# Optimization experiments

Hardware: AMD Instinct MI355X
Metric: run time of the kernel (lower is better)

Reference implementation:

```python
import jax, jax.numpy as jnp
import numpy as np

D_QK = 32  # out_channels // 8


def conv1x1(x, w, b):
    # x: [B,C,H,W], w: [O,C], b: [O] -> [B,O,H,W]
    return jnp.einsum('bchw,oc->bohw', x, w) + b[None, :, None, None]


def setup_inputs() -> dict:
    key = jax.random.key(0)
    ks = jax.random.split(key, 10)
    B, C, H, W = 4, 256, 64, 64
    in_ch, out_ch, attn_ch = 512, 256, 256
    s_in = 1.0 / np.sqrt(in_ch)
    s_at = 1.0 / np.sqrt(attn_ch)
    return {
        'ef': jax.random.normal(ks[0], (B, C, H, W), jnp.float32),
        'sf': jax.random.normal(ks[1], (B, C, H, W), jnp.float32),
        'Attn': jax.random.normal(ks[2], (B, attn_ch, H, W), jnp.float32),
        'Qw': jax.random.uniform(ks[3], (D_QK, in_ch), jnp.float32, -s_in, s_in),
        'Qb': jax.random.uniform(ks[4], (D_QK,), jnp.float32, -s_in, s_in),
        'Kw': jax.random.uniform(ks[5], (D_QK, attn_ch), jnp.float32, -s_at, s_at),
        'Kb': jax.random.uniform(ks[6], (D_QK,), jnp.float32, -s_at, s_at),
        'Vw': jax.random.uniform(ks[7], (out_ch, in_ch), jnp.float32, -s_in, s_in),
        'Vb': jax.random.uniform(ks[8], (out_ch,), jnp.float32, -s_in, s_in),
        'gamma': jnp.ones((1,), jnp.float32) * 0.25,
    }


def reference(ef, sf, Attn, Qw, Qb, Kw, Kb, Vw, Vb, gamma):
    B, C, H, W = ef.shape
    N = H * W
    x = jnp.concatenate((ef, sf), axis=1)  # [B, 2C, H, W]
    q = conv1x1(x, Qw, Qb).reshape(B, D_QK, N)         # [B, d, N]
    k = conv1x1(Attn, Kw, Kb).reshape(B, D_QK, N)      # [B, d, N]
    # scores[b, m, n] = sum_d q[b, d, m] * k[b, d, n]  (no 1/sqrt(d) scale)
    scores = jnp.einsum('bdm,bdn->bmn', q, k)
    attn = jax.nn.softmax(scores, axis=-1)             # [B, N, N]
    v = conv1x1(x, Vw, Vb).reshape(B, C, N)            # [B, C, N]
    # out[b, c, m] = sum_n v[b, c, n] * attn[b, m, n]
    out = jnp.einsum('bcn,bmn->bcm', v, attn).reshape(B, C, H, W)
    return gamma[0] * out + ef
```

## Files before the change

kernel.cpp:

```cpp
#include <hip/hip_runtime.h>
#include <hip/hip_bf16.h>

typedef short bf16x8 __attribute__((ext_vector_type(8)));
typedef float f32x4 __attribute__((ext_vector_type(4)));

#define MFMA16(a, b, c) __builtin_amdgcn_mfma_f32_16x16x32_bf16(a, b, c, 0, 0, 0)

#define NB 4
#define NC 256
#define NSP 4096
#define LOG2E 1.4426950408889634f

__device__ __forceinline__ unsigned short f2bf(float f) {
    return (unsigned short)((__float_as_uint(f) + 0x8000u) >> 16);
}
__device__ __forceinline__ unsigned pk2bf(float hi, float lo) {
    return __builtin_amdgcn_perm(__float_as_uint(hi) + 0x8000u,
                                 __float_as_uint(lo) + 0x8000u, 0x07060302u);
}

__global__ __launch_bounds__(256) void prep(
    const float* __restrict__ ef, const float* __restrict__ sf,
    const float* __restrict__ attn,
    const float* __restrict__ Qw, const float* __restrict__ Kw,
    const float* __restrict__ Vw,
    unsigned short* __restrict__ xt, unsigned short* __restrict__ at,
    unsigned short* __restrict__ Qwbf, unsigned short* __restrict__ Kwbf,
    unsigned short* __restrict__ Vwbf)
{
    __shared__ float tile[64][65];
    int gid = blockIdx.x;
    int t = threadIdx.x;

    if (gid >= 3072) {
        int i = (gid - 3072) * 256 + t;
        {
            const float4* vs = (const float4*)(Vw + (size_t)i * 8);
            float4 a = vs[0], c = vs[1];
            int4 st;
            st.x = (int)pk2bf(a.y, a.x); st.y = (int)pk2bf(a.w, a.z);
            st.z = (int)pk2bf(c.y, c.x); st.w = (int)pk2bf(c.w, c.z);
            *(int4*)(Vwbf + (size_t)i * 8) = st;
        }
        if (i < 2048) {
            const float4* qs = (const float4*)(Qw + (size_t)i * 8);
            float4 a = qs[0], c = qs[1];
            int4 st;
            st.x = (int)pk2bf(a.y, a.x); st.y = (int)pk2bf(a.w, a.z);
            st.z = (int)pk2bf(c.y, c.x); st.w = (int)pk2bf(c.w, c.z);
            *(int4*)(Qwbf + (size_t)i * 8) = st;
        }
        if (i < 1024) {
            const float4* ks = (const float4*)(Kw + (size_t)i * 8);
            float4 a = ks[0], c = ks[1];
            int4 st;
            st.x = (int)pk2bf(a.y, a.x); st.y = (int)pk2bf(a.w, a.z);
            st.z = (int)pk2bf(c.y, c.x); st.w = (int)pk2bf(c.w, c.z);
            *(int4*)(Kwbf + (size_t)i * 8) = st;
        }
        return;
    }

    const float* src; unsigned short* dst;
    int mt, cdst0, CW;
    if (gid < 2048) {
        int b = gid >> 9, r = gid & 511;
        mt = r >> 3; int ct = r & 7;
        src = (ct < 4 ? ef : sf) + ((size_t)(b * NC) + (ct & 3) * 64) * NSP;
        dst = xt + (size_t)b * NSP * 512; cdst0 = ct * 64; CW = 512;
    } else {
        int g2 = gid - 2048;
        int b = g2 >> 8, r = g2 & 255;
        mt = r >> 2; int ct = r & 3;
        src = attn + ((size_t)(b * NC) + ct * 64) * NSP;
        dst = at + (size_t)b * NSP * 256; cdst0 = ct * 64; CW = 256;
    }
    int m0 = mt * 64;
    int ml = t & 63, cl = t >> 6;
#pragma unroll
    for (int r = 0; r < 16; ++r)
        tile[ml][r * 4 + cl] = src[(size_t)(r * 4 + cl) * NSP + m0 + ml];
    __syncthreads();
    int cp = t & 31, mw = t >> 5;
#pragma unroll
    for (int r = 0; r < 8; ++r) {
        int m_l = r * 8 + mw;
        float v0 = tile[m_l][2 * cp], v1 = tile[m_l][2 * cp + 1];
        *(unsigned*)(dst + (size_t)(m0 + m_l) * CW + cdst0 + 2 * cp) = pk2bf(v1, v0);
    }
}

__global__ __launch_bounds__(256, 4) void proj(
    const unsigned short* __restrict__ xt, const unsigned short* __restrict__ at,
    const unsigned short* __restrict__ Qwbf, const unsigned short* __restrict__ Kwbf,
    const unsigned short* __restrict__ Vwbf,
    const float* __restrict__ Qb, const float* __restrict__ Kb,
    const float* __restrict__ Vb,
    unsigned short* __restrict__ qws, unsigned short* __restrict__ kws,
    unsigned short* __restrict__ vws)
{
    int bi = blockIdx.x;
    int t = threadIdx.x;
    int w = t >> 6, lane = t & 63, quad = lane >> 4, l15 = lane & 15;
    f32x4 zero = {0.f, 0.f, 0.f, 0.f};

    if (bi < 256) {
        int b = bi >> 6, m = (bi & 63) * 64 + w * 16;
        f32x4 a0 = zero, a1 = zero;
        const unsigned short* xrow = xt + ((size_t)(b * NSP) + m + l15) * 512;
#pragma unroll 4
        for (int ks = 0; ks < 16; ++ks) {
            bf16x8 af = *(const bf16x8*)(xrow + ks * 32 + quad * 8);
            bf16x8 b0 = *(const bf16x8*)(Qwbf + (size_t)l15 * 512 + ks * 32 + quad * 8);
            bf16x8 b1 = *(const bf16x8*)(Qwbf + (size_t)(16 + l15) * 512 + ks * 32 + quad * 8);
            a0 = MFMA16(af, b0, a0);
            a1 = MFMA16(af, b1, a1);
        }
        float bq0 = Qb[l15], bq1 = Qb[16 + l15];
#pragma unroll
        for (int r = 0; r < 4; ++r) {
            size_t mr = (size_t)(b * NSP) + m + quad * 4 + r;
            qws[mr * 32 + l15]      = f2bf((a0[r] + bq0) * LOG2E);
            qws[mr * 32 + 16 + l15] = f2bf((a1[r] + bq1) * LOG2E);
        }
    } else if (bi < 512) {
        int r2 = bi - 256;
        int b = r2 >> 6, m = (r2 & 63) * 64 + w * 16;
        f32x4 a0 = zero, a1 = zero;
        const unsigned short* arow = at + ((size_t)(b * NSP) + m + l15) * 256;
#pragma unroll 4
        for (int ks = 0; ks < 8; ++ks) {
            bf16x8 af = *(const bf16x8*)(arow + ks * 32 + quad * 8);
            bf16x8 b0 = *(const bf16x8*)(Kwbf + (size_t)l15 * 256 + ks * 32 + quad * 8);
            bf16x8 b1 = *(const bf16x8*)(Kwbf + (size_t)(16 + l15) * 256 + ks * 32 + quad * 8);
            a0 = MFMA16(af, b0, a0);
            a1 = MFMA16(af, b1, a1);
        }
        float bk0 = Kb[l15], bk1 = Kb[16 + l15];
#pragma unroll
        for (int r = 0; r < 4; ++r) {
            size_t mr = (size_t)(b * NSP) + m + quad * 4 + r;
            kws[mr * 32 + l15]      = f2bf(a0[r] + bk0);
            kws[mr * 32 + 16 + l15] = f2bf(a1[r] + bk1);
        }
    } else {
        int r2 = bi - 512;
        int mt = r2 & 127, coh = (r2 >> 7) & 1, b = r2 >> 8;
        int m0 = mt * 32;
        int co0 = coh * 128 + w * 32;

        f32x4 acc[2][2];
        acc[0][0] = zero; acc[0][1] = zero; acc[1][0] = zero; acc[1][1] = zero;

        const unsigned short* x0 = xt + ((size_t)(b * NSP) + m0 + l15) * 512;
        const unsigned short* x1 = x0 + 16 * 512;
        const unsigned short* vw0 = Vwbf + (size_t)(co0 + l15) * 512;
        const unsigned short* vw1 = Vwbf + (size_t)(co0 + 16 + l15) * 512;
#pragma unroll 4
        for (int ks = 0; ks < 16; ++ks) {
            bf16x8 a0 = *(const bf16x8*)(x0 + ks * 32 + quad * 8);
            bf16x8 a1 = *(const bf16x8*)(x1 + ks * 32 + quad * 8);
            bf16x8 b0 = *(const bf16x8*)(vw0 + ks * 32 + quad * 8);
            bf16x8 b1 = *(const bf16x8*)(vw1 + ks * 32 + quad * 8);
            acc[0][0] = MFMA16(a0, b0, acc[0][0]);
            acc[0][1] = MFMA16(a0, b1, acc[0][1]);
            acc[1][0] = MFMA16(a1, b0, acc[1][0]);
            acc[1][1] = MFMA16(a1, b1, acc[1][1]);
        }
#pragma unroll
        for (int mi = 0; mi < 2; ++mi)
#pragma unroll
            for (int ci = 0; ci < 2; ++ci) {
                int co = co0 + ci * 16 + l15;
                float bias = Vb[co];
                unsigned short* vp = vws + ((size_t)(b * 128 + mt) * 256 + co) * 32;
#pragma unroll
                for (int r = 0; r < 4; ++r)
                    vp[2 * (quad * 4 + r) + mi] = f2bf(acc[mi][ci][r] + bias);
            }
    }
}

__global__ __launch_bounds__(512, 2) void attention(
    const unsigned short* __restrict__ qws, const unsigned short* __restrict__ kws,
    const unsigned short* __restrict__ vws, const float* __restrict__ ef,
    const float* __restrict__ gamma, float* __restrict__ out)
{
    __shared__ unsigned short Plds[2][2][64 * 72];
    __shared__ float mrg[256][68];
    __shared__ float denl[2][64];

    int t = threadIdx.x;
    int g = t >> 8, tl = t & 255;
    int w = tl >> 6, lane = tl & 63, quad = lane >> 4, l15 = lane & 15;
    int b = blockIdx.x >> 6, m0 = (blockIdx.x & 63) << 6;

    const unsigned short* kbase = kws + (size_t)(b * NSP) * 32;
    const unsigned short* vbase = vws + (size_t)(b * 128) * 8192;

    bf16x8 qf = *(const bf16x8*)(qws + ((size_t)(b * NSP) + m0 + w * 16 + l15) * 32 + quad * 8);

    f32x4 zero = {0.f, 0.f, 0.f, 0.f};
    f32x4 acc[4][4];
#pragma unroll
    for (int i = 0; i < 4; ++i)
#pragma unroll
        for (int j = 0; j < 4; ++j) acc[i][j] = zero;
    float lp0 = 0.f, lp1 = 0.f, lp2 = 0.f, lp3 = 0.f;

    int tt0 = g * 64;
    bf16x8 kf[4];
#pragma unroll
    for (int j = 0; j < 4; ++j)
        kf[j] = *(const bf16x8*)(kbase + (size_t)((tt0 + (j >> 1)) * 32 + (j & 1) * 16 + l15) * 32 + quad * 8);
    bf16x8 vf[2][4];
#pragma unroll
    for (int h = 0; h < 2; ++h)
#pragma unroll
        for (int cc = 0; cc < 4; ++cc)
            vf[h][cc] = *(const bf16x8*)(vbase + (size_t)(tt0 + h) * 8192 + (w * 64 + cc * 16 + l15) * 32 + quad * 8);

    for (int it = 0; it < 32; ++it) {
        int buf = it & 1;
        f32x4 s0 = MFMA16(qf, kf[0], zero);
        f32x4 s1 = MFMA16(qf, kf[1], zero);
        f32x4 s2 = MFMA16(qf, kf[2], zero);
        f32x4 s3 = MFMA16(qf, kf[3], zero);

        float e0[4], e1[4], e2[4], e3[4];
#pragma unroll
        for (int r = 0; r < 4; ++r) {
            e0[r] = __builtin_amdgcn_exp2f(s0[r]);
            e1[r] = __builtin_amdgcn_exp2f(s1[r]);
            e2[r] = __builtin_amdgcn_exp2f(s2[r]);
            e3[r] = __builtin_amdgcn_exp2f(s3[r]);
        }
        lp0 += (e0[0] + e1[0]) + (e2[0] + e3[0]);
        lp1 += (e0[1] + e1[1]) + (e2[1] + e3[1]);
        lp2 += (e0[2] + e1[2]) + (e2[2] + e3[2]);
        lp3 += (e0[3] + e1[3]) + (e2[3] + e3[3]);

        unsigned short* pd = &Plds[g][buf][(w * 16 + quad * 4) * 72 + 2 * l15];
#pragma unroll
        for (int r = 0; r < 4; ++r) {
            *(unsigned*)(pd + r * 72)      = pk2bf(e1[r], e0[r]);
            *(unsigned*)(pd + r * 72 + 32) = pk2bf(e3[r], e2[r]);
        }

        int itn = it + 1 < 32 ? it + 1 : 31;
        int ttn = tt0 + 2 * itn;
#pragma unroll
        for (int j = 0; j < 4; ++j)
            kf[j] = *(const bf16x8*)(kbase + (size_t)((ttn + (j >> 1)) * 32 + (j & 1) * 16 + l15) * 32 + quad * 8);
        bf16x8 vfn[2][4];
#pragma unroll
        for (int h = 0; h < 2; ++h)
#pragma unroll
            for (int cc = 0; cc < 4; ++cc)
                vfn[h][cc] = *(const bf16x8*)(vbase + (size_t)(ttn + h) * 8192 + (w * 64 + cc * 16 + l15) * 32 + quad * 8);

        __syncthreads();

#pragma unroll
        for (int h = 0; h < 2; ++h) {
            bf16x8 pa0 = *(const bf16x8*)&Plds[g][buf][(0  + l15) * 72 + h * 32 + quad * 8];
            bf16x8 pa1 = *(const bf16x8*)&Plds[g][buf][(16 + l15) * 72 + h * 32 + quad * 8];
            bf16x8 pa2 = *(const bf16x8*)&Plds[g][buf][(32 + l15) * 72 + h * 32 + quad * 8];
            bf16x8 pa3 = *(const bf16x8*)&Plds[g][buf][(48 + l15) * 72 + h * 32 + quad * 8];
#pragma unroll
            for (int cc = 0; cc < 4; ++cc) {
                acc[0][cc] = MFMA16(pa0, vf[h][cc], acc[0][cc]);
                acc[1][cc] = MFMA16(pa1, vf[h][cc], acc[1][cc]);
                acc[2][cc] = MFMA16(pa2, vf[h][cc], acc[2][cc]);
                acc[3][cc] = MFMA16(pa3, vf[h][cc], acc[3][cc]);
            }
        }
#pragma unroll
        for (int h = 0; h < 2; ++h)
#pragma unroll
            for (int cc = 0; cc < 4; ++cc) vf[h][cc] = vfn[h][cc];
    }

    lp0 += __shfl_xor(lp0, 1); lp0 += __shfl_xor(lp0, 2); lp0 += __shfl_xor(lp0, 4); lp0 += __shfl_xor(lp0, 8);
    lp1 += __shfl_xor(lp1, 1); lp1 += __shfl_xor(lp1, 2); lp1 += __shfl_xor(lp1, 4); lp1 += __shfl_xor(lp1, 8);
    lp2 += __shfl_xor(lp2, 1); lp2 += __shfl_xor(lp2, 2); lp2 += __shfl_xor(lp2, 4); lp2 += __shfl_xor(lp2, 8);
    lp3 += __shfl_xor(lp3, 1); lp3 += __shfl_xor(lp3, 2); lp3 += __shfl_xor(lp3, 4); lp3 += __shfl_xor(lp3, 8);
    if (l15 == 0) {
        int base = w * 16 + quad * 4;
        denl[g][base + 0] = lp0; denl[g][base + 1] = lp1;
        denl[g][base + 2] = lp2; denl[g][base + 3] = lp3;
    }
    if (g == 1) {
#pragma unroll
        for (int qc = 0; qc < 4; ++qc)
#pragma unroll
            for (int cc = 0; cc < 4; ++cc)
                *(f32x4*)&mrg[w * 64 + cc * 16 + l15][qc * 16 + quad * 4] = acc[qc][cc];
    }
    __syncthreads();

    if (g == 0) {
        float gam = gamma[0];
#pragma unroll
        for (int qc = 0; qc < 4; ++qc) {
            int qb = qc * 16 + quad * 4;
            float4 d0 = *(const float4*)&denl[0][qb];
            float4 d1 = *(const float4*)&denl[1][qb];
            float r0 = gam / (d0.x + d1.x), r1 = gam / (d0.y + d1.y);
            float r2 = gam / (d0.z + d1.z), r3 = gam / (d0.w + d1.w);
#pragma unroll
            for (int cc = 0; cc < 4; ++cc) {
                int ch = w * 64 + cc * 16 + l15;
                f32x4 part = *(const f32x4*)&mrg[ch][qb];
                size_t off = ((size_t)(b * NC + ch)) * NSP + m0 + qb;
                float4 e = *(const float4*)(ef + off);
                float4 o;
                o.x = (acc[qc][cc][0] + part[0]) * r0 + e.x;
                o.y = (acc[qc][cc][1] + part[1]) * r1 + e.y;
                o.z = (acc[qc][cc][2] + part[2]) * r2 + e.z;
                o.w = (acc[qc][cc][3] + part[3]) * r3 + e.w;
                *(float4*)(out + off) = o;
            }
        }
    }
}

extern "C" void kernel_launch(void* const* d_in, const int* in_sizes, int n_in,
                              void* d_out, int out_size, void* d_ws, size_t ws_size,
                              hipStream_t stream) {
    const float* ef    = (const float*)d_in[0];
    const float* sf    = (const float*)d_in[1];
    const float* attn  = (const float*)d_in[2];
    const float* Qw    = (const float*)d_in[3];
    const float* Qb    = (const float*)d_in[4];
    const float* Kw    = (const float*)d_in[5];
    const float* Kb    = (const float*)d_in[6];
    const float* Vw    = (const float*)d_in[7];
    const float* Vb    = (const float*)d_in[8];
    const float* gamma = (const float*)d_in[9];
    float* out = (float*)d_out;

    unsigned short* qws  = (unsigned short*)d_ws;
    unsigned short* kws  = qws + (size_t)4 * 4096 * 32;
    unsigned short* vws  = kws + (size_t)4 * 4096 * 32;
    unsigned short* xt   = vws + (size_t)4 * 128 * 256 * 32;
    unsigned short* at   = xt  + (size_t)4 * 4096 * 512;
    unsigned short* Qwbf = at  + (size_t)4 * 4096 * 256;
    unsigned short* Kwbf = Qwbf + 32 * 512;
    unsigned short* Vwbf = Kwbf + 32 * 256;

    hipLaunchKernelGGL(prep, dim3(3136), dim3(256), 0, stream,
                       ef, sf, attn, Qw, Kw, Vw, xt, at, Qwbf, Kwbf, Vwbf);
    hipLaunchKernelGGL(proj, dim3(1536), dim3(256), 0, stream,
                       xt, at, Qwbf, Kwbf, Vwbf, Qb, Kb, Vb, qws, kws, vws);
    hipLaunchKernelGGL(attention, dim3(256), dim3(512), 0, stream,
                       qws, kws, vws, ef, gamma, out);
}
```

Before: 198.0 us.

## Fuse input transpose and bf16 conversion into Q/K/V projection kernels

Removes the separate prep pass that transposed ef/sf/Attn into bf16 workspace buffers. The Q, K and V projection kernels now read the fp32 inputs directly, transpose and convert them through a small LDS tile, and feed MFMA. This saves a full round trip of the transposed activations through global memory. In exchange ef/sf are read twice (by proj_q and proj_v), there are more kernel launches, and the blocks are small with only 512 blocks each.

```diff
diff --git a/kernel.cpp b/kernel.cpp
--- a/kernel.cpp
+++ b/kernel.cpp
@@ -19,165 +19,181 @@
                                  __float_as_uint(lo) + 0x8000u, 0x07060302u);
 }
 
-__global__ __launch_bounds__(256) void prep(
-    const float* __restrict__ ef, const float* __restrict__ sf,
-    const float* __restrict__ attn,
+__global__ __launch_bounds__(256) void prep_w(
     const float* __restrict__ Qw, const float* __restrict__ Kw,
     const float* __restrict__ Vw,
-    unsigned short* __restrict__ xt, unsigned short* __restrict__ at,
     unsigned short* __restrict__ Qwbf, unsigned short* __restrict__ Kwbf,
     unsigned short* __restrict__ Vwbf)
 {
-    __shared__ float tile[64][65];
-    int gid = blockIdx.x;
-    int t = threadIdx.x;
-
-    if (gid >= 3072) {
-        int i = (gid - 3072) * 256 + t;
-        {
-            const float4* vs = (const float4*)(Vw + (size_t)i * 8);
-            float4 a = vs[0], c = vs[1];
-            int4 st;
-            st.x = (int)pk2bf(a.y, a.x); st.y = (int)pk2bf(a.w, a.z);
-            st.z = (int)pk2bf(c.y, c.x); st.w = (int)pk2bf(c.w, c.z);
-            *(int4*)(Vwbf + (size_t)i * 8) = st;
-        }
-        if (i < 2048) {
-            const float4* qs = (const float4*)(Qw + (size_t)i * 8);
-            float4 a = qs[0], c = qs[1];
-            int4 st;
-            st.x = (int)pk2bf(a.y, a.x); st.y = (int)pk2bf(a.w, a.z);
-            st.z = (int)pk2bf(c.y, c.x); st.w = (int)pk2bf(c.w, c.z);
-            *(int4*)(Qwbf + (size_t)i * 8) = st;
-        }
-        if (i < 1024) {
-            const float4* ks = (const float4*)(Kw + (size_t)i * 8);
-            float4 a = ks[0], c = ks[1];
-            int4 st;
-            st.x = (int)pk2bf(a.y, a.x); st.y = (int)pk2bf(a.w, a.z);
-            st.z = (int)pk2bf(c.y, c.x); st.w = (int)pk2bf(c.w, c.z);
-            *(int4*)(Kwbf + (size_t)i * 8) = st;
-        }
-        return;
-    }
-
-    const float* src; unsigned short* dst;
-    int mt, cdst0, CW;
-    if (gid < 2048) {
-        int b = gid >> 9, r = gid & 511;
-        mt = r >> 3; int ct = r & 7;
-        src = (ct < 4 ? ef : sf) + ((size_t)(b * NC) + (ct & 3) * 64) * NSP;
-        dst = xt + (size_t)b * NSP * 512; cdst0 = ct * 64; CW = 512;
-    } else {
-        int g2 = gid - 2048;
-        int b = g2 >> 8, r = g2 & 255;
-        mt = r >> 2; int ct = r & 3;
-        src = attn + ((size_t)(b * NC) + ct * 64) * NSP;
-        dst = at + (size_t)b * NSP * 256; cdst0 = ct * 64; CW = 256;
-    }
-    int m0 = mt * 64;
-    int ml = t & 63, cl = t >> 6;
-#pragma unroll
-    for (int r = 0; r < 16; ++r)
-        tile[ml][r * 4 + cl] = src[(size_t)(r * 4 + cl) * NSP + m0 + ml];
-    __syncthreads();
-    int cp = t & 31, mw = t >> 5;
-#pragma unroll
-    for (int r = 0; r < 8; ++r) {
-        int m_l = r * 8 + mw;
-        float v0 = tile[m_l][2 * cp], v1 = tile[m_l][2 * cp + 1];
-        *(unsigned*)(dst + (size_t)(m0 + m_l) * CW + cdst0 + 2 * cp) = pk2bf(v1, v0);
-    }
-}
-
-__global__ __launch_bounds__(256, 4) void proj(
-    const unsigned short* __restrict__ xt, const unsigned short* __restrict__ at,
-    const unsigned short* __restrict__ Qwbf, const unsigned short* __restrict__ Kwbf,
-    const unsigned short* __restrict__ Vwbf,
-    const float* __restrict__ Qb, const float* __restrict__ Kb,
-    const float* __restrict__ Vb,
-    unsigned short* __restrict__ qws, unsigned short* __restrict__ kws,
-    unsigned short* __restrict__ vws)
-{
-    int bi = blockIdx.x;
+    int i = blockIdx.x * 256 + threadIdx.x;
+    {
+        const float4* vs = (const float4*)(Vw + (size_t)i * 8);
+        float4 a = vs[0], c = vs[1];
+        int4 st;
+        st.x = (int)pk2bf(a.y, a.x); st.y = (int)pk2bf(a.w, a.z);
+        st.z = (int)pk2bf(c.y, c.x); st.w = (int)pk2bf(c.w, c.z);
+        *(int4*)(Vwbf + (size_t)i * 8) = st;
+    }
+    if (i < 2048) {
+        const float4* qs = (const float4*)(Qw + (size_t)i * 8);
+        float4 a = qs[0], c = qs[1];
+        int4 st;
+        st.x = (int)pk2bf(a.y, a.x); st.y = (int)pk2bf(a.w, a.z);
+        st.z = (int)pk2bf(c.y, c.x); st.w = (int)pk2bf(c.w, c.z);
+        *(int4*)(Qwbf + (size_t)i * 8) = st;
+    }
+    if (i < 1024) {
+        const float4* ks = (const float4*)(Kw + (size_t)i * 8);
+        float4 a = ks[0], c = ks[1];
+        int4 st;
+        st.x = (int)pk2bf(a.y, a.x); st.y = (int)pk2bf(a.w, a.z);
+        st.z = (int)pk2bf(c.y, c.x); st.w = (int)pk2bf(c.w, c.z);
+        *(int4*)(Kwbf + (size_t)i * 8) = st;
+    }
+}
+
+__global__ __launch_bounds__(256) void proj_q(
+    const float* __restrict__ ef, const float* __restrict__ sf,
+    const unsigned short* __restrict__ Qwbf, const float* __restrict__ Qb,
+    unsigned short* __restrict__ qws)
+{
+    __shared__ __align__(16) unsigned short xt[32][72];
+
     int t = threadIdx.x;
     int w = t >> 6, lane = t & 63, quad = lane >> 4, l15 = lane & 15;
+    int mt = blockIdx.x, b = blockIdx.y, m0 = mt * 32;
+    int ci = t & 63, sm = t >> 6;
+    int mi = w >> 1, oh = w & 1;
+
+    f32x4 acc = {0.f, 0.f, 0.f, 0.f};
+
+    for (int c = 0; c < 8; ++c) {
+        const float* src = (c < 4 ? ef : sf) +
+                           ((size_t)(b * NC) + (c & 3) * 64 + ci) * NSP + m0 + sm * 8;
+        float4 x0 = *(const float4*)src;
+        float4 x1 = *(const float4*)(src + 4);
+        __syncthreads();
+        unsigned short* xd = &xt[sm * 8][ci];
+        xd[0]   = f2bf(x0.x); xd[72]  = f2bf(x0.y);
+        xd[144] = f2bf(x0.z); xd[216] = f2bf(x0.w);
+        xd[288] = f2bf(x1.x); xd[360] = f2bf(x1.y);
+        xd[432] = f2bf(x1.z); xd[504] = f2bf(x1.w);
+        __syncthreads();
+        int ci0 = c * 64;
+#pragma unroll
+        for (int ks = 0; ks < 2; ++ks) {
+            bf16x8 a  = *(const bf16x8*)&xt[mi * 16 + l15][ks * 32 + quad * 8];
+            bf16x8 bq = *(const bf16x8*)(Qwbf + (size_t)(oh * 16 + l15) * 512 + ci0 + ks * 32 + quad * 8);
+            acc = MFMA16(a, bq, acc);
+        }
+    }
+
+    int o = oh * 16 + l15;
+    float bb = Qb[o];
+#pragma unroll
+    for (int r = 0; r < 4; ++r) {
+        int m = m0 + mi * 16 + quad * 4 + r;
+        qws[((size_t)(b * NSP) + m) * 32 + o] = f2bf((acc[r] + bb) * LOG2E);
+    }
+}
+
+__global__ __launch_bounds__(256) void proj_k(
+    const float* __restrict__ attn,
+    const unsigned short* __restrict__ Kwbf, const float* __restrict__ Kb,
+    unsigned short* __restrict__ kws)
+{
+    __shared__ __align__(16) unsigned short xt[32][72];
+
+    int t = threadIdx.x;
+    int w = t >> 6, lane = t & 63, quad = lane >> 4, l15 = lane & 15;
+    int mt = blockIdx.x, b = blockIdx.y, m0 = mt * 32;
+    int ci = t & 63, sm = t >> 6;
+    int mi = w >> 1, oh = w & 1;
+
+    f32x4 acc = {0.f, 0.f, 0.f, 0.f};
+
+    for (int c = 0; c < 4; ++c) {
+        const float* src = attn + ((size_t)(b * NC) + c * 64 + ci) * NSP + m0 + sm * 8;
+        float4 x0 = *(const float4*)src;
+        float4 x1 = *(const float4*)(src + 4);
+        __syncthreads();
+        unsigned short* xd = &xt[sm * 8][ci];
+        xd[0]   = f2bf(x0.x); xd[72]  = f2bf(x0.y);
+        xd[144] = f2bf(x0.z); xd[216] = f2bf(x0.w);
+        xd[288] = f2bf(x1.x); xd[360] = f2bf(x1.y);
+        xd[432] = f2bf(x1.z); xd[504] = f2bf(x1.w);
+        __syncthreads();
+        int ci0 = c * 64;
+#pragma unroll
+        for (int ks = 0; ks < 2; ++ks) {
+            bf16x8 a  = *(const bf16x8*)&xt[mi * 16 + l15][ks * 32 + quad * 8];
+            bf16x8 bk = *(const bf16x8*)(Kwbf + (size_t)(oh * 16 + l15) * 256 + ci0 + ks * 32 + quad * 8);
+            acc = MFMA16(a, bk, acc);
+        }
+    }
+
+    int o = oh * 16 + l15;
+    float bb = Kb[o];
+#pragma unroll
+    for (int r = 0; r < 4; ++r) {
+        int m = m0 + mi * 16 + quad * 4 + r;
+        kws[((size_t)(b * NSP) + m) * 32 + o] = f2bf(acc[r] + bb);
+    }
+}
+
+__global__ __launch_bounds__(256) void proj_v(
+    const float* __restrict__ ef, const float* __restrict__ sf,
+    const unsigned short* __restrict__ Vwbf, const float* __restrict__ Vb,
+    unsigned short* __restrict__ vws)
+{
+    __shared__ __align__(16) unsigned short xt[32][72];
+
+    int t = threadIdx.x;
+    int w = t >> 6, lane = t & 63, quad = lane >> 4, l15 = lane & 15;
+    int mt = blockIdx.x, b = blockIdx.y, m0 = mt * 32;
+    int ci = t & 63, sm = t >> 6;
+
     f32x4 zero = {0.f, 0.f, 0.f, 0.f};
-
-    if (bi < 256) {
-        int b = bi >> 6, m = (bi & 63) * 64 + w * 16;
-        f32x4 a0 = zero, a1 = zero;
-        const unsigned short* xrow = xt + ((size_t)(b * NSP) + m + l15) * 512;
-#pragma unroll 4
-        for (int ks = 0; ks < 16; ++ks) {
-            bf16x8 af = *(const bf16x8*)(xrow + ks * 32 + quad * 8);
-            bf16x8 b0 = *(const bf16x8*)(Qwbf + (size_t)l15 * 512 + ks * 32 + quad * 8);
-            bf16x8 b1 = *(const bf16x8*)(Qwbf + (size_t)(16 + l15) * 512 + ks * 32 + quad * 8);
-            a0 = MFMA16(af, b0, a0);
-            a1 = MFMA16(af, b1, a1);
-        }
-        float bq0 = Qb[l15], bq1 = Qb[16 + l15];
-#pragma unroll
-        for (int r = 0; r < 4; ++r) {
-            size_t mr = (size_t)(b * NSP) + m + quad * 4 + r;
-            qws[mr * 32 + l15]      = f2bf((a0[r] + bq0) * LOG2E);
-            qws[mr * 32 + 16 + l15] = f2bf((a1[r] + bq1) * LOG2E);
-        }
-    } else if (bi < 512) {
-        int r2 = bi - 256;
-        int b = r2 >> 6, m = (r2 & 63) * 64 + w * 16;
-        f32x4 a0 = zero, a1 = zero;
-        const unsigned short* arow = at + ((size_t)(b * NSP) + m + l15) * 256;
-#pragma unroll 4
-        for (int ks = 0; ks < 8; ++ks) {
-            bf16x8 af = *(const bf16x8*)(arow + ks * 32 + quad * 8);
-            bf16x8 b0 = *(const bf16x8*)(Kwbf + (size_t)l15 * 256 + ks * 32 + quad * 8);
-            bf16x8 b1 = *(const bf16x8*)(Kwbf + (size_t)(16 + l15) * 256 + ks * 32 + quad * 8);
-            a0 = MFMA16(af, b0, a0);
-            a1 = MFMA16(af, b1, a1);
-        }
-        float bk0 = Kb[l15], bk1 = Kb[16 + l15];
-#pragma unroll
-        for (int r = 0; r < 4; ++r) {
-            size_t mr = (size_t)(b * NSP) + m + quad * 4 + r;
-            kws[mr * 32 + l15]      = f2bf(a0[r] + bk0);
-            kws[mr * 32 + 16 + l15] = f2bf(a1[r] + bk1);
-        }
-    } else {
-        int r2 = bi - 512;
-        int mt = r2 & 127, coh = (r2 >> 7) & 1, b = r2 >> 8;
-        int m0 = mt * 32;
-        int co0 = coh * 128 + w * 32;
-
-        f32x4 acc[2][2];
-        acc[0][0] = zero; acc[0][1] = zero; acc[1][0] = zero; acc[1][1] = zero;
-
-        const unsigned short* x0 = xt + ((size_t)(b * NSP) + m0 + l15) * 512;
-        const unsigned short* x1 = x0 + 16 * 512;
-        const unsigned short* vw0 = Vwbf + (size_t)(co0 + l15) * 512;
-        const unsigned short* vw1 = Vwbf + (size_t)(co0 + 16 + l15) * 512;
-#pragma unroll 4
-        for (int ks = 0; ks < 16; ++ks) {
-            bf16x8 a0 = *(const bf16x8*)(x0 + ks * 32 + quad * 8);
-            bf16x8 a1 = *(const bf16x8*)(x1 + ks * 32 + quad * 8);
-            bf16x8 b0 = *(const bf16x8*)(vw0 + ks * 32 + quad * 8);
-            bf16x8 b1 = *(const bf16x8*)(vw1 + ks * 32 + quad * 8);
-            acc[0][0] = MFMA16(a0, b0, acc[0][0]);
-            acc[0][1] = MFMA16(a0, b1, acc[0][1]);
-            acc[1][0] = MFMA16(a1, b0, acc[1][0]);
-            acc[1][1] = MFMA16(a1, b1, acc[1][1]);
-        }
-#pragma unroll
-        for (int mi = 0; mi < 2; ++mi)
-#pragma unroll
-            for (int ci = 0; ci < 2; ++ci) {
-                int co = co0 + ci * 16 + l15;
-                float bias = Vb[co];
-                unsigned short* vp = vws + ((size_t)(b * 128 + mt) * 256 + co) * 32;
-#pragma unroll
-                for (int r = 0; r < 4; ++r)
-                    vp[2 * (quad * 4 + r) + mi] = f2bf(acc[mi][ci][r] + bias);
+    f32x4 acc[2][4];
+#pragma unroll
+    for (int mi = 0; mi < 2; ++mi)
+#pragma unroll
+        for (int ot = 0; ot < 4; ++ot) acc[mi][ot] = zero;
+
+    for (int c = 0; c < 8; ++c) {
+        const float* src = (c < 4 ? ef : sf) +
+                           ((size_t)(b * NC) + (c & 3) * 64 + ci) * NSP + m0 + sm * 8;
+        float4 x0 = *(const float4*)src;
+        float4 x1 = *(const float4*)(src + 4);
+        __syncthreads();
+        unsigned short* xd = &xt[sm * 8][ci];
+        xd[0]   = f2bf(x0.x); xd[72]  = f2bf(x0.y);
+        xd[144] = f2bf(x0.z); xd[216] = f2bf(x0.w);
+        xd[288] = f2bf(x1.x); xd[360] = f2bf(x1.y);
+        xd[432] = f2bf(x1.z); xd[504] = f2bf(x1.w);
+        __syncthreads();
+        int ci0 = c * 64;
+#pragma unroll
+        for (int ks = 0; ks < 2; ++ks) {
+            bf16x8 a0 = *(const bf16x8*)&xt[l15][ks * 32 + quad * 8];
+            bf16x8 a1 = *(const bf16x8*)&xt[16 + l15][ks * 32 + quad * 8];
+#pragma unroll
+            for (int ot = 0; ot < 4; ++ot) {
+                bf16x8 bv = *(const bf16x8*)(Vwbf + (size_t)(w * 64 + ot * 16 + l15) * 512 + ci0 + ks * 32 + quad * 8);
+                acc[0][ot] = MFMA16(a0, bv, acc[0][ot]);
+                acc[1][ot] = MFMA16(a1, bv, acc[1][ot]);
             }
+        }
+    }
+
+#pragma unroll
+    for (int ot = 0; ot < 4; ++ot) {
+        int ch = w * 64 + ot * 16 + l15;
+        float bias = Vb[ch];
+        unsigned* vp = (unsigned*)(vws + ((size_t)((b * 128 + mt) * 256 + ch)) * 32);
+#pragma unroll
+        for (int r = 0; r < 4; ++r)
+            vp[quad * 4 + r] = pk2bf(acc[1][ot][r] + bias, acc[0][ot][r] + bias);
     }
 }
 
@@ -343,16 +359,18 @@
     unsigned short* qws  = (unsigned short*)d_ws;
     unsigned short* kws  = qws + (size_t)4 * 4096 * 32;
     unsigned short* vws  = kws + (size_t)4 * 4096 * 32;
-    unsigned short* xt   = vws + (size_t)4 * 128 * 256 * 32;
-    unsigned short* at   = xt  + (size_t)4 * 4096 * 512;
-    unsigned short* Qwbf = at  + (size_t)4 * 4096 * 256;
+    unsigned short* Qwbf = vws + (size_t)4 * 128 * 256 * 32;
     unsigned short* Kwbf = Qwbf + 32 * 512;
     unsigned short* Vwbf = Kwbf + 32 * 256;
 
-    hipLaunchKernelGGL(prep, dim3(3136), dim3(256), 0, stream,
-                       ef, sf, attn, Qw, Kw, Vw, xt, at, Qwbf, Kwbf, Vwbf);
-    hipLaunchKernelGGL(proj, dim3(1536), dim3(256), 0, stream,
-                       xt, at, Qwbf, Kwbf, Vwbf, Qb, Kb, Vb, qws, kws, vws);
+    hipLaunchKernelGGL(prep_w, dim3(64), dim3(256), 0, stream,
+                       Qw, Kw, Vw, Qwbf, Kwbf, Vwbf);
+    hipLaunchKernelGGL(proj_q, dim3(128, 4), dim3(256), 0, stream,
+                       ef, sf, Qwbf, Qb, qws);
+    hipLaunchKernelGGL(proj_k, dim3(128, 4), dim3(256), 0, stream,
+                       attn, Kwbf, Kb, kws);
+    hipLaunchKernelGGL(proj_v, dim3(128, 4), dim3(256), 0, stream,
+                       ef, sf, Vwbf, Vb, vws);
     hipLaunchKernelGGL(attention, dim3(256), dim3(512), 0, stream,
                        qws, kws, vws, ef, gamma, out);
 }
```

Result: faster. 193.8 us (-2.1%).
